# Kernel tuning notes

Hardware: AMD Instinct MI355X
Metric: run time of the kernel (lower is better)

The kernel has to match this reference:

```python
import jax, jax.numpy as jnp
import numpy as np

EMBED_DIM = 2048
NUM_HEADS = 16
BLOCK_SIZE = 128


def setup_inputs() -> dict:
    key = jax.random.key(0)
    k1, k2, k3 = jax.random.split(key, 3)
    B, S, E = 2, 4096, EMBED_DIM
    x = jax.random.normal(k1, (B, S, E), dtype=jnp.float32)
    # small init so attention logits are in a sane range
    w_qkv = jax.random.normal(k2, (3 * E, E), dtype=jnp.float32) * 0.02
    w_out = jax.random.normal(k3, (E, E), dtype=jnp.float32) * 0.02
    b_out = jnp.zeros((E,), dtype=jnp.float32)
    return {"x": x, "w_qkv": w_qkv, "w_out": w_out, "b_out": b_out}


def _flash_attention_v2(q, k, v, block_size, scale):
    # q,k,v: [B,H,S,D]; S divisible by block_size.
    # Faithful to the torch module, including its extra l_ij factor in the
    # output rescaling (out += beta*l_ij/l_new * (p @ v)).
    B, H, S, D = q.shape
    nb = S // block_size
    qb = q.reshape(B, H, nb, block_size, D)          # all query blocks at once
    kb = k.reshape(B, H, nb, block_size, D).transpose(2, 0, 1, 3, 4)  # [nb,B,H,bs,D]
    vb = v.reshape(B, H, nb, block_size, D).transpose(2, 0, 1, 3, 4)

    out0 = jnp.zeros_like(qb)
    l0 = jnp.zeros((B, H, nb, block_size, 1), dtype=q.dtype)
    m0 = jnp.full((B, H, nb, block_size, 1), -jnp.inf, dtype=q.dtype)

    def step(carry, kv):
        out, l, m = carry
        k_j, v_j = kv  # [B,H,bs,D]
        s = jnp.einsum('bhnqd,bhkd->bhnqk', qb, k_j) * scale  # [B,H,nb,bs,bs]
        m_ij = jnp.max(s, axis=-1, keepdims=True)
        p = jnp.exp(s - m_ij)
        l_ij = jnp.sum(p, axis=-1, keepdims=True)
        m_new = jnp.maximum(m, m_ij)
        alpha = jnp.exp(m - m_new)
        beta = jnp.exp(m_ij - m_new)
        l_new = alpha * l + beta * l_ij
        pv = jnp.einsum('bhnqk,bhkd->bhnqd', p, v_j)
        out_new = (alpha * l / l_new) * out + (beta * l_ij / l_new) * pv
        return (out_new, l_new, m_new), None

    (out, _, _), _ = jax.lax.scan(step, (out0, l0, m0), (kb, vb))
    return out.reshape(B, H, S, D)


def reference(x, w_qkv, w_out, b_out):
    B, S, E = x.shape
    H = NUM_HEADS
    D = E // H
    scale = 1.0 / np.sqrt(D).astype(np.float32)
    qkv = (x @ w_qkv.T).reshape(B, S, 3, H, D)
    q, k, v = jnp.moveaxis(qkv, 2, 0)            # each [B,S,H,D]
    q = q.transpose(0, 2, 1, 3)                   # [B,H,S,D]
    k = k.transpose(0, 2, 1, 3)
    v = v.transpose(0, 2, 1, 3)
    out = _flash_attention_v2(q, k, v, BLOCK_SIZE, scale)  # [B,H,S,D]
    out = out.transpose(0, 2, 1, 3).reshape(B, S, E)
    return out @ w_out.T + b_out
```

## Files before the change

kernel.cpp:

```cpp
#include <hip/hip_runtime.h>
#include <hip/hip_bf16.h>
#include <stdint.h>

#define DEV __device__ __forceinline__

typedef __attribute__((ext_vector_type(8))) short short8;
typedef __attribute__((ext_vector_type(4))) float f32x4;

#define B_ 2
#define S_ 4096
#define E_ 2048
#define H_ 16
#define D_ 128

#define BAR() asm volatile("s_barrier" ::: "memory")
#define LGKM0() asm volatile("s_waitcnt lgkmcnt(0)" ::: "memory")
#define VMC(N) asm volatile("s_waitcnt vmcnt(" #N ")" ::: "memory")

DEV unsigned short f2bf(float x) {
  union { float f; uint32_t u; } a; a.f = x;
  uint32_t r = a.u + 0x7fffu + ((a.u >> 16) & 1u);
  return (unsigned short)(r >> 16);
}

DEV unsigned int cvt_pk_bf16(float a, float b) {
  unsigned int r;
  asm("v_cvt_pk_bf16_f32 %0, %1, %2" : "=v"(r) : "v"(a), "v"(b));
  return r;
}

DEV float exp2f_(float x) { return __builtin_amdgcn_exp2f(x); }

DEV void glds16(const void* g, void* l) {
  __builtin_amdgcn_global_load_lds(
      (const __attribute__((address_space(1))) uint32_t*)g,
      (__attribute__((address_space(3))) uint32_t*)l, 16, 0, 0);
}

__global__ __launch_bounds__(256) void cvtk(const float* __restrict__ in,
                                            unsigned short* __restrict__ out, int n4) {
  int i = blockIdx.x * blockDim.x + threadIdx.x;
  int stride = gridDim.x * blockDim.x;
  for (; i < n4; i += stride) {
    float4 v = ((const float4*)in)[i];
    ushort4 o;
    o.x = f2bf(v.x); o.y = f2bf(v.y); o.z = f2bf(v.z); o.w = f2bf(v.w);
    ((ushort4*)out)[i] = o;
  }
}

template<int OUT_F32>
__global__ __launch_bounds__(512, 2) void gemm256(
    const unsigned short* __restrict__ A,
    const unsigned short* __restrict__ Bm,
    void* __restrict__ Cp,
    const float* __restrict__ bias,
    int M, int N, int K, int nbn)
{
  __shared__ __align__(16) unsigned char lds[131072];
  const int NT = K >> 6;
  const int K2 = K * 2;
  int cpx = gridDim.x >> 3;
  int bid = (blockIdx.x & 7) * cpx + (blockIdx.x >> 3);
  int bm = bid / nbn, bn = bid % nbn;
  int m0 = bm * 256, n0 = bn * 256;
  int t = threadIdx.x, lane = t & 63, wv = t >> 6;
  int lo = lane & 15, hi = lane >> 4;
  int wm = wv >> 2, wn = wv & 3;

  int colsw = ((t & 7) * 16) ^ (((t >> 3) & 7) << 4);
  const unsigned char* gA = (const unsigned char*)A + (size_t)(m0 + (t >> 3)) * K2 + colsw;
  const unsigned char* gB = (const unsigned char*)Bm + (size_t)(n0 + (t >> 3)) * K2 + colsw;

  int swzl = (lo & 7) << 4;
  int colk0 = (hi * 16) ^ swzl;
  int colk1 = (64 + hi * 16) ^ swzl;
  unsigned char* rdA = lds + wm * 16384 + lo * 128;
  unsigned char* rdB = lds + 32768 + (wn >> 1) * 16384 + ((wn & 1) * 64 + lo) * 128;

  f32x4 acc[8][4] = {};

  auto STG = [&](int isA, int d, int h, int kt) {
    if (kt >= NT) return;
    const unsigned char* g = (isA ? gA : gB) + (size_t)h * 128 * K2 + (size_t)kt * 128;
    unsigned char* l = lds + (isA ? 0 : 32768) + d * 65536 + h * 16384 + wv * 1024;
    glds16(g, l);
    glds16(g + (size_t)64 * K2, l + 8192);
  };
  auto DSA = [&](int d, int g4, int colk, short8* dst) {
#pragma unroll
    for (int i = 0; i < 4; ++i)
      dst[i] = *(const short8*)(rdA + d * 65536 + (g4 * 4 + i) * 2048 + colk);
  };
  auto DSB = [&](int d, int colk, short8* dst) {
#pragma unroll
    for (int i = 0; i < 4; ++i)
      dst[i] = *(const short8*)(rdB + d * 65536 + i * 2048 + colk);
  };
  auto MM = [&](int g4, short8* a, short8* b) {
    __builtin_amdgcn_s_setprio(1);
#pragma unroll
    for (int i = 0; i < 4; ++i)
#pragma unroll
      for (int j = 0; j < 4; ++j)
        acc[g4 * 4 + i][j] =
            __builtin_amdgcn_mfma_f32_16x16x32_bf16(a[i], b[j], acc[g4 * 4 + i][j], 0, 0, 0);
    __builtin_amdgcn_s_setprio(0);
  };

  STG(1, 0, 0, 0); STG(1, 0, 1, 0); STG(0, 0, 0, 0); STG(0, 0, 1, 0);
  STG(0, 1, 0, 1); STG(0, 1, 1, 1);
  VMC(4);
  BAR();

  short8 aT[4], aU[4], b0[4], b1[4];
  const int TL = (NT >> 1) - 1;
  for (int it = 0; it <= TL; ++it) {
    int j0 = 2 * it;
    DSA(0, 0, colk0, aT); DSB(0, colk0, b0);
    STG(1, 1, 0, j0 + 1);
    BAR(); MM(0, aT, b0); LGKM0(); BAR();
    DSA(0, 1, colk0, aU); DSB(0, colk1, b1);
    STG(1, 1, 1, j0 + 1);
    BAR(); MM(1, aU, b0); LGKM0(); BAR();
    DSA(0, 0, colk1, aT);
    STG(0, 0, 0, j0 + 2);
    BAR(); MM(0, aT, b1); LGKM0(); BAR();
    DSA(0, 1, colk1, aU);
    STG(0, 0, 1, j0 + 2);
    BAR(); MM(1, aU, b1); LGKM0();
    if (it == TL) { VMC(0); } else { VMC(4); }
    BAR();
    DSA(1, 0, colk0, aT); DSB(1, colk0, b0);
    STG(1, 0, 0, j0 + 2);
    BAR(); MM(0, aT, b0); LGKM0(); BAR();
    DSA(1, 1, colk0, aU); DSB(1, colk1, b1);
    STG(1, 0, 1, j0 + 2);
    BAR(); MM(1, aU, b0); LGKM0(); BAR();
    DSA(1, 0, colk1, aT);
    STG(0, 1, 0, j0 + 3);
    BAR(); MM(0, aT, b1); LGKM0(); BAR();
    DSA(1, 1, colk1, aU);
    STG(0, 1, 1, j0 + 3);
    BAR(); MM(1, aU, b1); LGKM0(); VMC(4);
    BAR();
  }

  if constexpr (OUT_F32) {
    float* C = (float*)Cp;
#pragma unroll
    for (int mf = 0; mf < 8; ++mf)
#pragma unroll
      for (int nf = 0; nf < 4; ++nf) {
        int row = m0 + wm * 128 + mf * 16 + hi * 4;
        int col = n0 + wn * 64 + nf * 16 + lo;
        float bv = bias[col];
#pragma unroll
        for (int r = 0; r < 4; ++r)
          C[(size_t)(row + r) * N + col] = acc[mf][nf][r] + bv;
      }
  } else {
    unsigned short* C = (unsigned short*)Cp;
#pragma unroll
    for (int mf = 0; mf < 8; ++mf)
#pragma unroll
      for (int nf = 0; nf < 4; ++nf) {
        int row = m0 + wm * 128 + mf * 16 + hi * 4;
        int col = n0 + wn * 64 + nf * 16 + lo;
#pragma unroll
        for (int r = 0; r < 4; ++r)
          C[(size_t)(row + r) * N + col] = f2bf(acc[mf][nf][r]);
      }
  }
}

__global__ __launch_bounds__(256) void transpose_v(const unsigned short* __restrict__ qkv,
                                                   unsigned short* __restrict__ vt) {
  __shared__ __align__(16) unsigned char tl[32768];
  int bid = blockIdx.x;
  int st = bid & 31, bh = bid >> 5;
  int h = bh & 15, b = bh >> 4;
  int s0 = st * 128;
  int t = threadIdx.x, c = t & 15, rr = t >> 4;
#pragma unroll
  for (int i = 0; i < 8; ++i) {
    int s = rr + i * 16;
    const unsigned short* g = qkv + ((((size_t)b * S_ + s0 + s) * 3 + 2) * H_ + h) * D_ + c * 8;
    *(uint4*)(tl + s * 256 + ((c * 16) ^ (((s >> 3) & 7) << 4))) = *(const uint4*)g;
  }
  __syncthreads();
#pragma unroll
  for (int i = 0; i < 8; ++i) {
    int d = rr + i * 16;
    unsigned int w[4];
#pragma unroll
    for (int jj = 0; jj < 4; ++jj) {
      int s_a = c * 8 + jj * 2;
      unsigned int u0 = *(const unsigned short*)(tl + s_a * 256 + ((d * 2) ^ ((c & 7) << 4)));
      unsigned int u1 = *(const unsigned short*)(tl + (s_a + 1) * 256 + ((d * 2) ^ ((c & 7) << 4)));
      w[jj] = u0 | (u1 << 16);
    }
    uint4 val; val.x = w[0]; val.y = w[1]; val.z = w[2]; val.w = w[3];
    unsigned short* g = vt + (((size_t)b * H_ + h) * D_ + d) * S_ + s0 + c * 8;
    *(uint4*)g = val;
  }
}

__global__ __launch_bounds__(512, 2) void attn_fwd(
    const unsigned short* __restrict__ qkv,
    const unsigned short* __restrict__ vt,
    unsigned short* __restrict__ abuf)
{
  __shared__ __align__(16) unsigned char lds[65536];
  unsigned char* lK = lds;
  unsigned char* lV = lds + 32768;

  int bid = (blockIdx.x & 7) * 64 + (blockIdx.x >> 3);
  int qb = bid & 15, bh = bid >> 4;
  int h = bh & 15, b = bh >> 4;
  int t = threadIdx.x, lane = t & 63, wv = t >> 6;
  int hi = lane >> 4, lo = lane & 15;
  int q0 = qb * 256;
  const float c1 = 0.12751744f;

  short8 qf[2][4];
#pragma unroll
  for (int qj = 0; qj < 2; ++qj) {
    const unsigned short* qbase =
        qkv + ((((size_t)b * S_ + q0 + wv * 32 + qj * 16 + lo) * 3 + 0) * H_ + h) * D_;
#pragma unroll
    for (int ks = 0; ks < 4; ++ks)
      qf[qj][ks] = *(const short8*)(qbase + ks * 32 + hi * 8);
  }

  int sw = ((t & 15) * 16) ^ (((t >> 4) & 7) << 4);
  const unsigned char* gkb =
      (const unsigned char*)(qkv + (((size_t)b * S_ * 3 + 1) * H_ + h) * D_) +
      (size_t)(t >> 4) * 12288 + sw;
  const unsigned char* gvb =
      (const unsigned char*)(vt + ((size_t)b * H_ + h) * D_ * S_) +
      (size_t)(t >> 4) * 8192 + sw;
  unsigned char* lkd = lK + wv * 1024;
  unsigned char* lvd = lV + wv * 1024;

  f32x4 oacc[8][2] = {};
  float m_run[2] = {-__builtin_inff(), -__builtin_inff()};
  float l_run[2] = {0.f, 0.f};
  union PW { unsigned int u[4]; short8 s; };
  PW pp[2][4];

#pragma unroll
  for (int i = 0; i < 4; ++i) {
    glds16(gkb + i * 393216, lkd + i * 8192);
    glds16(gvb + i * 262144, lvd + i * 8192);
  }

  for (int jb = 0; jb < 32; ++jb) {
    VMC(0);
    BAR();

    f32x4 sacc[8][2];
    __builtin_amdgcn_s_setprio(1);
#pragma unroll
    for (int kf = 0; kf < 8; ++kf) {
      int kvr = kf * 16 + lo;
      int swz = (kvr & 7) << 4;
      sacc[kf][0] = f32x4{0.f, 0.f, 0.f, 0.f};
      sacc[kf][1] = f32x4{0.f, 0.f, 0.f, 0.f};
#pragma unroll
      for (int ks = 0; ks < 4; ++ks) {
        short8 kfr = *(const short8*)(lK + kvr * 256 + ((ks * 64 + hi * 16) ^ swz));
        sacc[kf][0] = __builtin_amdgcn_mfma_f32_16x16x32_bf16(kfr, qf[0][ks], sacc[kf][0], 0, 0, 0);
        sacc[kf][1] = __builtin_amdgcn_mfma_f32_16x16x32_bf16(kfr, qf[1][ks], sacc[kf][1], 0, 0, 0);
      }
    }
    __builtin_amdgcn_s_setprio(0);

    float m2[2], li[2], coef[2];
#pragma unroll
    for (int qj = 0; qj < 2; ++qj) {
      float mloc = -__builtin_inff();
#pragma unroll
      for (int kf = 0; kf < 8; ++kf)
#pragma unroll
        for (int r = 0; r < 4; ++r) mloc = fmaxf(mloc, sacc[kf][qj][r]);
      mloc = fmaxf(mloc, __shfl_xor(mloc, 16));
      mloc = fmaxf(mloc, __shfl_xor(mloc, 32));
      m2[qj] = mloc * c1;
      float lloc = 0.f;
#pragma unroll
      for (int kf = 0; kf < 8; ++kf)
#pragma unroll
        for (int r = 0; r < 4; ++r) {
          float p = exp2f_(fmaf(sacc[kf][qj][r], c1, -m2[qj]));
          sacc[kf][qj][r] = p;
          lloc += p;
        }
      lloc += __shfl_xor(lloc, 16);
      lloc += __shfl_xor(lloc, 32);
      li[qj] = lloc;
    }

    if (__all(m2[0] <= m_run[0] && m2[1] <= m_run[1])) {
#pragma unroll
      for (int qj = 0; qj < 2; ++qj) {
        coef[qj] = exp2f_(m2[qj] - m_run[qj]) * li[qj];
        l_run[qj] += coef[qj];
      }
    } else {
      float alpha[2];
#pragma unroll
      for (int qj = 0; qj < 2; ++qj) {
        float mn = fmaxf(m_run[qj], m2[qj]);
        alpha[qj] = exp2f_(m_run[qj] - mn);
        coef[qj] = exp2f_(m2[qj] - mn) * li[qj];
        l_run[qj] = alpha[qj] * l_run[qj] + coef[qj];
        m_run[qj] = mn;
      }
#pragma unroll
      for (int df = 0; df < 8; ++df)
#pragma unroll
        for (int qj = 0; qj < 2; ++qj)
#pragma unroll
          for (int r = 0; r < 4; ++r) oacc[df][qj][r] *= alpha[qj];
    }

#pragma unroll
    for (int qj = 0; qj < 2; ++qj) {
      float cf = coef[qj];
#pragma unroll
      for (int ks = 0; ks < 4; ++ks) {
        unsigned int a0 = cvt_pk_bf16(sacc[2 * ks][qj][0] * cf, sacc[2 * ks][qj][1] * cf);
        unsigned int b0 = cvt_pk_bf16(sacc[2 * ks + 1][qj][0] * cf, sacc[2 * ks + 1][qj][1] * cf);
        unsigned int a1 = cvt_pk_bf16(sacc[2 * ks][qj][2] * cf, sacc[2 * ks][qj][3] * cf);
        unsigned int b1 = cvt_pk_bf16(sacc[2 * ks + 1][qj][2] * cf, sacc[2 * ks + 1][qj][3] * cf);
        asm("v_permlane32_swap_b32 %0, %1" : "+v"(a0), "+v"(b0));
        asm("v_permlane16_swap_b32 %0, %1" : "+v"(a0), "+v"(b0));
        asm("v_permlane32_swap_b32 %0, %1" : "+v"(a1), "+v"(b1));
        asm("v_permlane16_swap_b32 %0, %1" : "+v"(a1), "+v"(b1));
        pp[qj][ks].u[0] = a0;
        pp[qj][ks].u[1] = a1;
        pp[qj][ks].u[2] = b0;
        pp[qj][ks].u[3] = b1;
      }
    }

    __builtin_amdgcn_s_setprio(1);
#pragma unroll
    for (int ks = 0; ks < 4; ++ks) {
#pragma unroll
      for (int df = 0; df < 8; ++df) {
        int dr = df * 16 + lo;
        short8 vf = *(const short8*)(lV + dr * 256 + ((ks * 64 + hi * 16) ^ ((dr & 7) << 4)));
        oacc[df][0] = __builtin_amdgcn_mfma_f32_16x16x32_bf16(vf, pp[0][ks].s, oacc[df][0], 0, 0, 0);
        oacc[df][1] = __builtin_amdgcn_mfma_f32_16x16x32_bf16(vf, pp[1][ks].s, oacc[df][1], 0, 0, 0);
      }
    }
    __builtin_amdgcn_s_setprio(0);

    BAR();
    if (jb < 31) {
      size_t kvK = (size_t)(jb + 1) * 1572864;
      size_t kvV = (size_t)(jb + 1) * 256;
#pragma unroll
      for (int i = 0; i < 4; ++i) {
        glds16(gkb + kvK + i * 393216, lkd + i * 8192);
        glds16(gvb + kvV + i * 262144, lvd + i * 8192);
      }
    }
  }

  BAR();
#pragma unroll
  for (int qj = 0; qj < 2; ++qj) {
    int rq = wv * 32 + qj * 16 + lo;
    int swzq = (rq & 7) << 4;
    float inv = 1.0f / l_run[qj];
#pragma unroll
    for (int df = 0; df < 8; ++df) {
      uint2 pk;
      pk.x = cvt_pk_bf16(oacc[df][qj][0] * inv, oacc[df][qj][1] * inv);
      pk.y = cvt_pk_bf16(oacc[df][qj][2] * inv, oacc[df][qj][3] * inv);
      *(uint2*)(lds + rq * 256 + ((df * 32 + hi * 8) ^ swzq)) = pk;
    }
  }
  __syncthreads();
#pragma unroll
  for (int i = 0; i < 8; ++i) {
    int row = i * 32 + (t >> 4);
    int c = t & 15;
    uint4 val = *(const uint4*)(lds + row * 256 + ((c * 16) ^ ((row & 7) << 4)));
    unsigned short* dst = abuf + (((size_t)b * S_ + q0 + row) * H_ + h) * D_ + c * 8;
    *(uint4*)dst = val;
  }
}

extern "C" void kernel_launch(void* const* d_in, const int* in_sizes, int n_in,
                              void* d_out, int out_size, void* d_ws, size_t ws_size,
                              hipStream_t stream) {
  const float* x = (const float*)d_in[0];
  const float* w_qkv = (const float*)d_in[1];
  const float* w_out = (const float*)d_in[2];
  const float* b_out = (const float*)d_in[3];
  float* out = (float*)d_out;
  char* ws = (char*)d_ws;

  unsigned short* xb    = (unsigned short*)(ws);
  unsigned short* wqkvb = (unsigned short*)(ws + 33554432);
  unsigned short* woutb = (unsigned short*)(ws + 58720256);
  unsigned short* qkvb  = (unsigned short*)(ws + 67108864);
  unsigned short* vtb   = (unsigned short*)(ws + 167772160);
  unsigned short* abuf  = xb;

  cvtk<<<2048, 256, 0, stream>>>(x, xb, (B_ * S_ * E_) / 4);
  cvtk<<<2048, 256, 0, stream>>>(w_qkv, wqkvb, (3 * E_ * E_) / 4);
  cvtk<<<1024, 256, 0, stream>>>(w_out, woutb, (E_ * E_) / 4);

  gemm256<0><<<768, 512, 0, stream>>>(xb, wqkvb, (void*)qkvb, nullptr,
                                      B_ * S_, 3 * E_, E_, 24);
  transpose_v<<<1024, 256, 0, stream>>>(qkvb, vtb);
  attn_fwd<<<512, 512, 0, stream>>>(qkvb, vtb, abuf);
  gemm256<1><<<256, 512, 0, stream>>>(abuf, woutb, (void*)out, b_out,
                                      B_ * S_, E_, E_, 8);
}
```

Baseline: 637.6 us.

## Software-pipeline attention loop with double-buffered V and fuse bf16 conversion kernels

Restructures the attention main loop so the P·V MFMAs for the previous KV block run right after the Q·K MFMAs of the current block. V tiles are double-buffered in LDS so the next block's loads can be issued while the current P is still being packed. The aim is to hide softmax latency behind matrix work and shorten the serial dependency within each iteration. LDS per block grows from 64 KB to 96 KB, which may cut resident blocks per CU and work against the launch bound of 2. Separately, the three fp32-to-bf16 conversion launches are merged into one kernel to save launch overhead.

```diff
diff --git a/kernel.cpp b/kernel.cpp
--- a/kernel.cpp
+++ b/kernel.cpp
@@ -37,15 +37,24 @@
       (__attribute__((address_space(3))) uint32_t*)l, 16, 0, 0);
 }
 
-__global__ __launch_bounds__(256) void cvtk(const float* __restrict__ in,
-                                            unsigned short* __restrict__ out, int n4) {
+__global__ __launch_bounds__(256) void cvtk3(
+    const float* __restrict__ x, const float* __restrict__ wq,
+    const float* __restrict__ wo, unsigned short* __restrict__ xb,
+    unsigned short* __restrict__ wqb, unsigned short* __restrict__ wob) {
+  const int n1 = (B_ * S_ * E_) / 4, n2 = (3 * E_ * E_) / 4, n3 = (E_ * E_) / 4;
   int i = blockIdx.x * blockDim.x + threadIdx.x;
   int stride = gridDim.x * blockDim.x;
-  for (; i < n4; i += stride) {
-    float4 v = ((const float4*)in)[i];
+  for (; i < n1 + n2 + n3; i += stride) {
+    const float4* s;
+    ushort4* d;
+    int j;
+    if (i < n1) { s = (const float4*)x; d = (ushort4*)xb; j = i; }
+    else if (i < n1 + n2) { s = (const float4*)wq; d = (ushort4*)wqb; j = i - n1; }
+    else { s = (const float4*)wo; d = (ushort4*)wob; j = i - n1 - n2; }
+    float4 v = s[j];
     ushort4 o;
     o.x = f2bf(v.x); o.y = f2bf(v.y); o.z = f2bf(v.z); o.w = f2bf(v.w);
-    ((ushort4*)out)[i] = o;
+    d[j] = o;
   }
 }
 
@@ -211,9 +220,8 @@
     const unsigned short* __restrict__ vt,
     unsigned short* __restrict__ abuf)
 {
-  __shared__ __align__(16) unsigned char lds[65536];
+  __shared__ __align__(16) unsigned char lds[98304];
   unsigned char* lK = lds;
-  unsigned char* lV = lds + 32768;
 
   int bid = (blockIdx.x & 7) * 64 + (blockIdx.x >> 3);
   int qb = bid & 15, bh = bid >> 4;
@@ -241,25 +249,27 @@
       (const unsigned char*)(vt + ((size_t)b * H_ + h) * D_ * S_) +
       (size_t)(t >> 4) * 8192 + sw;
   unsigned char* lkd = lK + wv * 1024;
-  unsigned char* lvd = lV + wv * 1024;
 
   f32x4 oacc[8][2] = {};
   float m_run[2] = {-__builtin_inff(), -__builtin_inff()};
   float l_run[2] = {0.f, 0.f};
+  f32x4 sacc[8][2];
   union PW { unsigned int u[4]; short8 s; };
   PW pp[2][4];
-
-#pragma unroll
-  for (int i = 0; i < 4; ++i) {
-    glds16(gkb + i * 393216, lkd + i * 8192);
-    glds16(gvb + i * 262144, lvd + i * 8192);
-  }
-
-  for (int jb = 0; jb < 32; ++jb) {
-    VMC(0);
-    BAR();
-
-    f32x4 sacc[8][2];
+  float coef[2];
+
+  auto STAGE = [&](int n) {
+    size_t kvK = (size_t)n * 1572864;
+    size_t kvV = (size_t)n * 256;
+    unsigned char* vd = lds + 32768 + ((n & 1) << 15) + wv * 1024;
+#pragma unroll
+    for (int i = 0; i < 4; ++i) {
+      glds16(gkb + kvK + i * 393216, lkd + i * 8192);
+      glds16(gvb + kvV + i * 262144, vd + i * 8192);
+    }
+  };
+
+  auto QK = [&]() {
     __builtin_amdgcn_s_setprio(1);
 #pragma unroll
     for (int kf = 0; kf < 8; ++kf) {
@@ -275,8 +285,23 @@
       }
     }
     __builtin_amdgcn_s_setprio(0);
-
-    float m2[2], li[2], coef[2];
+  };
+
+  auto PV = [&](const unsigned char* vb) {
+#pragma unroll
+    for (int ks = 0; ks < 4; ++ks) {
+#pragma unroll
+      for (int df = 0; df < 8; ++df) {
+        int dr = df * 16 + lo;
+        short8 vf = *(const short8*)(vb + dr * 256 + ((ks * 64 + hi * 16) ^ ((dr & 7) << 4)));
+        oacc[df][0] = __builtin_amdgcn_mfma_f32_16x16x32_bf16(vf, pp[0][ks].s, oacc[df][0], 0, 0, 0);
+        oacc[df][1] = __builtin_amdgcn_mfma_f32_16x16x32_bf16(vf, pp[1][ks].s, oacc[df][1], 0, 0, 0);
+      }
+    }
+  };
+
+  auto SOFTMAX = [&]() {
+    float m2[2], li[2];
 #pragma unroll
     for (int qj = 0; qj < 2; ++qj) {
       float mloc = -__builtin_inff();
@@ -300,7 +325,6 @@
       lloc += __shfl_xor(lloc, 32);
       li[qj] = lloc;
     }
-
     if (__all(m2[0] <= m_run[0] && m2[1] <= m_run[1])) {
 #pragma unroll
       for (int qj = 0; qj < 2; ++qj) {
@@ -324,7 +348,9 @@
 #pragma unroll
           for (int r = 0; r < 4; ++r) oacc[df][qj][r] *= alpha[qj];
     }
-
+  };
+
+  auto PACK = [&]() {
 #pragma unroll
     for (int qj = 0; qj < 2; ++qj) {
       float cf = coef[qj];
@@ -344,33 +370,29 @@
         pp[qj][ks].u[3] = b1;
       }
     }
-
-    __builtin_amdgcn_s_setprio(1);
-#pragma unroll
-    for (int ks = 0; ks < 4; ++ks) {
-#pragma unroll
-      for (int df = 0; df < 8; ++df) {
-        int dr = df * 16 + lo;
-        short8 vf = *(const short8*)(lV + dr * 256 + ((ks * 64 + hi * 16) ^ ((dr & 7) << 4)));
-        oacc[df][0] = __builtin_amdgcn_mfma_f32_16x16x32_bf16(vf, pp[0][ks].s, oacc[df][0], 0, 0, 0);
-        oacc[df][1] = __builtin_amdgcn_mfma_f32_16x16x32_bf16(vf, pp[1][ks].s, oacc[df][1], 0, 0, 0);
-      }
-    }
-    __builtin_amdgcn_s_setprio(0);
-
+  };
+
+  STAGE(0);
+  VMC(0);
+  BAR();
+  QK();
+  SOFTMAX();
+  BAR();
+  STAGE(1);
+  PACK();
+
+  for (int jb = 1; jb < 32; ++jb) {
+    VMC(0);
     BAR();
-    if (jb < 31) {
-      size_t kvK = (size_t)(jb + 1) * 1572864;
-      size_t kvV = (size_t)(jb + 1) * 256;
-#pragma unroll
-      for (int i = 0; i < 4; ++i) {
-        glds16(gkb + kvK + i * 393216, lkd + i * 8192);
-        glds16(gvb + kvV + i * 262144, lvd + i * 8192);
-      }
-    }
-  }
-
-  BAR();
+    QK();
+    PV(lds + 32768 + (((jb - 1) & 1) << 15));
+    SOFTMAX();
+    BAR();
+    if (jb < 31) STAGE(jb + 1);
+    PACK();
+  }
+  PV(lds + 65536);
+
 #pragma unroll
   for (int qj = 0; qj < 2; ++qj) {
     int rq = wv * 32 + qj * 16 + lo;
@@ -412,9 +434,7 @@
   unsigned short* vtb   = (unsigned short*)(ws + 167772160);
   unsigned short* abuf  = xb;
 
-  cvtk<<<2048, 256, 0, stream>>>(x, xb, (B_ * S_ * E_) / 4);
-  cvtk<<<2048, 256, 0, stream>>>(w_qkv, wqkvb, (3 * E_ * E_) / 4);
-  cvtk<<<1024, 256, 0, stream>>>(w_out, woutb, (E_ * E_) / 4);
+  cvtk3<<<2048, 256, 0, stream>>>(x, w_qkv, w_out, xb, wqkvb, woutb);
 
   gemm256<0><<<768, 512, 0, stream>>>(xb, wqkvb, (void*)qkvb, nullptr,
                                       B_ * S_, 3 * E_, E_, 24);
```

New measurement: 710.9 us. 11.5% more time.
